# Kernel tuning notes

Hardware: AMD Instinct MI355X
Metric: run time of the kernel (lower is better)

## Reference

```python
import jax, jax.numpy as jnp
import numpy as np
from jax import lax

B, T, S = 8, 4096, 64  # batch, time steps, hidden states


def setup_inputs() -> dict:
    key = jax.random.key(0)
    k1, k2 = jax.random.split(key)
    # log-domain pairwise factors: log_factors[b, t, i, j] = log p(z_{t+1}=j, x_t | z_t=i)
    log_factors = jax.random.normal(k1, (B, T, S, S), dtype=jnp.float32)
    # initial log factor over the first state
    log_init = jax.random.normal(k2, (B, S), dtype=jnp.float32)
    return {"log_factors": log_factors, "log_init": log_init}


def reference(log_factors, log_init):
    """HMM forward algorithm: sequential logaddexp/add chain reduction over time.

    Equivalent to sequential_sum_product(logaddexp, add, log_factors, 'time')
    followed by adding log_init over 'state' and reducing all with logaddexp.
    Implemented as the O(T*S^2) alpha-recursion (vector carry) rather than the
    O(T*S^3) matrix chain -- same math, efficient form.
    """
    fs = jnp.moveaxis(log_factors, 1, 0)  # [T, B, S, S]

    def step(alpha, f_t):
        # alpha: [B, S] over state i ; f_t: [B, S, S] over (i, j)
        alpha_next = jax.nn.logsumexp(alpha[:, :, None] + f_t, axis=1)  # [B, S]
        return alpha_next, None

    alpha_T, _ = lax.scan(step, log_init, fs)
    return jax.nn.logsumexp(alpha_T, axis=-1)  # [B] log-normalizer
```

## Files before the change

kernel.cpp:

```cpp
#include <hip/hip_runtime.h>


#define HMM_B 8
#define HMM_T 4096
#define HMM_S 64
#define HMM_C 128
#define HMM_L (HMM_T / HMM_C)

typedef __attribute__((ext_vector_type(8))) short s16x8;
typedef __attribute__((ext_vector_type(4))) float f32x4;
typedef __attribute__((ext_vector_type(4))) unsigned int u32x4;

__device__ inline void gld16(const float* g, const float* l) {
  __builtin_amdgcn_global_load_lds((const __attribute__((address_space(1))) void*)g,
                                   (__attribute__((address_space(3))) void*)l, 16, 0, 0);
}

__device__ inline unsigned cvtpk(float lo, float hi) {
  unsigned r;
  asm("v_cvt_pk_bf16_f32 %0, %1, %2" : "=v"(r) : "v"(lo), "v"(hi));
  return r;
}

__device__ inline float dpp_fmax16(float x) {
  int xi = __float_as_int(x);
  x = fmaxf(x, __int_as_float(__builtin_amdgcn_mov_dpp(xi, 0xB1, 0xF, 0xF, 1)));
  xi = __float_as_int(x);
  x = fmaxf(x, __int_as_float(__builtin_amdgcn_mov_dpp(xi, 0x4E, 0xF, 0xF, 1)));
  xi = __float_as_int(x);
  x = fmaxf(x, __int_as_float(__builtin_amdgcn_mov_dpp(xi, 0x141, 0xF, 0xF, 1)));
  xi = __float_as_int(x);
  x = fmaxf(x, __int_as_float(__builtin_amdgcn_mov_dpp(xi, 0x140, 0xF, 0xF, 1)));
  return x;
}

__device__ inline float bflo(unsigned w) { return __uint_as_float(w << 16); }
__device__ inline float bfhi(unsigned w) { return __uint_as_float(w & 0xffff0000u); }


__global__ __launch_bounds__(256, 3)
void hmm_phase1(const float* __restrict__ lf, unsigned short* __restrict__ wsE,
                unsigned short* __restrict__ wsEt, float* __restrict__ wsM) {
  __shared__ struct {
    float fbuf[2][4096];
    unsigned short fB[4096];
    unsigned short escr[4][1408];
  } sm;

  const int tid = threadIdx.x;
  const int w   = tid >> 6;
  const int l   = tid & 63;
  const int wg  = blockIdx.x;
  const int bb  = wg >> 7;
  const int cc  = wg & (HMM_C - 1);
  const float* fbase = lf + ((size_t)(bb * HMM_T + cc * HMM_L)) * (HMM_S * HMM_S);

  auto issue = [&](int t) {
    const int par = t & 1;
    const float* fb = fbase + (size_t)t * 4096;
#pragma unroll
    for (int u = 0; u < 4; ++u) {
      int slot = (w * 4 + u) * 64 + l;
      int k    = slot >> 4;
      int q16  = slot & 15;
      const float* src = fb + k * 64 + ((q16 ^ (k & 7)) << 2);
      gld16(src, &sm.fbuf[par][(w * 4 + u) * 256]);
    }
  };

  issue(0);
  issue(1);

  float mracc0 = 0.f, mracc1 = 0.f, mracc2 = 0.f, mracc3 = 0.f;
  const int c4 = l & 15, q = l >> 4;

  for (int t = 0; t < HMM_L; ++t) {
    const int par = t & 1;

    if (t < HMM_L - 1) asm volatile("s_waitcnt vmcnt(4)" ::: "memory");
    else               asm volatile("s_waitcnt vmcnt(0)" ::: "memory");
    __builtin_amdgcn_sched_barrier(0);

#pragma unroll
    for (int u = 0; u < 2; ++u) {
      const int g = 2 * w + (l >> 5);
      const int j = (l & 31) + 32 * u;
      float v[8];
#pragma unroll
      for (int e = 0; e < 8; ++e) {
        int k = 8 * g + e;
        v[e] = sm.fbuf[par][k * 64 + (((j >> 2) ^ (k & 7)) << 2) + (j & 3)];
      }
      unsigned p0 = cvtpk(__expf(v[0]), __expf(v[1]));
      unsigned p1 = cvtpk(__expf(v[2]), __expf(v[3]));
      unsigned p2 = cvtpk(__expf(v[4]), __expf(v[5]));
      unsigned p3 = cvtpk(__expf(v[6]), __expf(v[7]));
      int slot = ((g >> 2) * 4 + (j >> 4)) * 64 + ((g & 3) << 4) + (j & 15);
      u32x4 o; o.x = p0; o.y = p1; o.z = p2; o.w = p3;
      *(u32x4*)&sm.fB[slot * 8] = o;
    }

    asm volatile("s_waitcnt lgkmcnt(0)" ::: "memory");
    __builtin_amdgcn_sched_barrier(0);
    __builtin_amdgcn_s_barrier();
    __builtin_amdgcn_sched_barrier(0);

    if (t + 2 < HMM_L) issue(t + 2);

    s16x8 a0, a1;
    if (t == 0) {
      const int iloc = 16 * w + (l & 15);
      const int kb0 = (l >> 4) * 8, kb1 = 32 + (l >> 4) * 8;
#pragma unroll
      for (int e = 0; e < 8; ++e) {
        a0[e] = (short)((kb0 + e == iloc) ? 0x3F80 : 0);
        a1[e] = (short)((kb1 + e == iloc) ? 0x3F80 : 0);
      }
    } else {
      a0 = *(const s16x8*)&sm.escr[w][(l & 15) * 88 + ((l >> 4) * 8)];
      a1 = *(const s16x8*)&sm.escr[w][(l & 15) * 88 + 32 + ((l >> 4) * 8)];
    }

    f32x4 acc[4];
#pragma unroll
    for (int n = 0; n < 4; ++n) {
      s16x8 b0 = *(const s16x8*)&sm.fB[((0 + n) * 64 + l) * 8];
      s16x8 b1 = *(const s16x8*)&sm.fB[((4 + n) * 64 + l) * 8];
      f32x4 c = {0.f, 0.f, 0.f, 0.f};
      c = __builtin_amdgcn_mfma_f32_16x16x32_bf16(a0, b0, c, 0, 0, 0);
      c = __builtin_amdgcn_mfma_f32_16x16x32_bf16(a1, b1, c, 0, 0, 0);
      acc[n] = c;
    }

    float inv[4];
    {
      float m0 = fmaxf(fmaxf(acc[0][0], acc[1][0]), fmaxf(acc[2][0], acc[3][0]));
      float m1 = fmaxf(fmaxf(acc[0][1], acc[1][1]), fmaxf(acc[2][1], acc[3][1]));
      float m2 = fmaxf(fmaxf(acc[0][2], acc[1][2]), fmaxf(acc[2][2], acc[3][2]));
      float m3 = fmaxf(fmaxf(acc[0][3], acc[1][3]), fmaxf(acc[2][3], acc[3][3]));
      m0 = dpp_fmax16(m0); m1 = dpp_fmax16(m1);
      m2 = dpp_fmax16(m2); m3 = dpp_fmax16(m3);
      mracc0 += __log2f(m0); mracc1 += __log2f(m1);
      mracc2 += __log2f(m2); mracc3 += __log2f(m3);
      inv[0] = __builtin_amdgcn_rcpf(m0); inv[1] = __builtin_amdgcn_rcpf(m1);
      inv[2] = __builtin_amdgcn_rcpf(m2); inv[3] = __builtin_amdgcn_rcpf(m3);
    }
#pragma unroll
    for (int n = 0; n < 4; ++n) {
      unsigned p0 = cvtpk(acc[n][0] * inv[0], acc[n][1] * inv[1]);
      unsigned p1 = cvtpk(acc[n][2] * inv[2], acc[n][3] * inv[3]);
      sm.escr[w][(4 * q + 0) * 88 + 16 * n + c4] = (unsigned short)(p0 & 0xffffu);
      sm.escr[w][(4 * q + 1) * 88 + 16 * n + c4] = (unsigned short)(p0 >> 16);
      sm.escr[w][(4 * q + 2) * 88 + 16 * n + c4] = (unsigned short)(p1 & 0xffffu);
      sm.escr[w][(4 * q + 3) * 88 + 16 * n + c4] = (unsigned short)(p1 >> 16);
    }

    asm volatile("s_waitcnt lgkmcnt(0)" ::: "memory");
    __builtin_amdgcn_sched_barrier(0);
    __builtin_amdgcn_s_barrier();
    __builtin_amdgcn_sched_barrier(0);
  }

  __syncthreads();

  {
    const size_t cb = ((size_t)(bb * HMM_C + cc)) * 4096;
    const int j = tid & 63, p4 = tid >> 6;
    unsigned short o0[8], o1[8];
#pragma unroll
    for (int rl = 0; rl < 8; ++rl)  o0[rl] = sm.escr[p4][rl * 88 + j];
#pragma unroll
    for (int rl = 0; rl < 8; ++rl)  o1[rl] = sm.escr[p4][(rl + 8) * 88 + j];
    *(u32x4*)&wsEt[cb + j * 64 + p4 * 16]     = *(u32x4*)o0;
    *(u32x4*)&wsEt[cb + j * 64 + p4 * 16 + 8] = *(u32x4*)o1;

    if ((cc & 15) == 0) {
      const int r = tid >> 2, jq = tid & 3;
      u32x4 v0 = *(const u32x4*)&sm.escr[r >> 4][(r & 15) * 88 + jq * 16];
      u32x4 v1 = *(const u32x4*)&sm.escr[r >> 4][(r & 15) * 88 + jq * 16 + 8];
      *(u32x4*)&wsE[cb + r * 64 + jq * 16]     = v0;
      *(u32x4*)&wsE[cb + r * 64 + jq * 16 + 8] = v1;
    }

    if (c4 == 0) {
      const float ln2 = 0.6931471805599453f;
      float* dst = wsM + (size_t)(bb * HMM_C + cc) * 64 + 16 * w + 4 * q;
      dst[0] = mracc0 * ln2; dst[1] = mracc1 * ln2;
      dst[2] = mracc2 * ln2; dst[3] = mracc3 * ln2;
    }
  }
}


__global__ __launch_bounds__(64)
void hmm_combine16(const unsigned short* __restrict__ inE,
                   const unsigned short* __restrict__ inEt,
                   const float* __restrict__ inM,
                   unsigned short* __restrict__ outEt,
                   float* __restrict__ outM) {
  __shared__ float sS[64];
  __shared__ float sM[64];
  __shared__ unsigned short pL[4096];

  const int l = threadIdx.x, c4 = l & 15, q = l >> 4;
  const int b = blockIdx.x >> 3, g = blockIdx.x & 7;
  const int cbase = b * HMM_C + g * 16;

  s16x8 afr[4][2];
#pragma unroll
  for (int m = 0; m < 4; ++m)
#pragma unroll
    for (int h = 0; h < 2; ++h)
      afr[m][h] = *(const s16x8*)&inE[(size_t)cbase * 4096 +
                                      (m * 16 + c4) * 64 + h * 32 + q * 8];
  sM[l] = inM[(size_t)cbase * 64 + l];

  u32x4 braw[2][4];
  float mv;
  {
    const unsigned short* Et = inEt + (size_t)(cbase + 1) * 4096;
#pragma unroll
    for (int h = 0; h < 2; ++h)
#pragma unroll
      for (int n = 0; n < 4; ++n)
        braw[h][n] = *(const u32x4*)&Et[(n * 16 + c4) * 64 + h * 32 + q * 8];
    mv = inM[(size_t)(cbase + 1) * 64 + l];
  }

  for (int c = 1; c < 16; ++c) {
    u32x4 bcur[2][4];
#pragma unroll
    for (int h = 0; h < 2; ++h)
#pragma unroll
      for (int n = 0; n < 4; ++n) bcur[h][n] = braw[h][n];
    float mcur = mv;
    if (c < 15) {
      const unsigned short* Et = inEt + (size_t)(cbase + c + 1) * 4096;
#pragma unroll
      for (int h = 0; h < 2; ++h)
#pragma unroll
        for (int n = 0; n < 4; ++n)
          braw[h][n] = *(const u32x4*)&Et[(n * 16 + c4) * 64 + h * 32 + q * 8];
      mv = inM[(size_t)(cbase + c + 1) * 64 + l];
    }

    float nu = mcur;
    nu = fmaxf(nu, __shfl_xor(nu, 1));  nu = fmaxf(nu, __shfl_xor(nu, 2));
    nu = fmaxf(nu, __shfl_xor(nu, 4));  nu = fmaxf(nu, __shfl_xor(nu, 8));
    nu = fmaxf(nu, __shfl_xor(nu, 16)); nu = fmaxf(nu, __shfl_xor(nu, 32));
    sS[l] = __expf(mcur - nu);

    s16x8 bfr[2][4];
#pragma unroll
    for (int h = 0; h < 2; ++h) {
      f32x4 s0 = *(const f32x4*)&sS[h * 32 + q * 8];
      f32x4 s1 = *(const f32x4*)&sS[h * 32 + q * 8 + 4];
#pragma unroll
      for (int n = 0; n < 4; ++n) {
        u32x4 raw = bcur[h][n];
        unsigned p0 = cvtpk(bflo(raw.x) * s0[0], bfhi(raw.x) * s0[1]);
        unsigned p1 = cvtpk(bflo(raw.y) * s0[2], bfhi(raw.y) * s0[3]);
        unsigned p2 = cvtpk(bflo(raw.z) * s1[0], bfhi(raw.z) * s1[1]);
        unsigned p3 = cvtpk(bflo(raw.w) * s1[2], bfhi(raw.w) * s1[3]);
        u32x4 o; o.x = p0; o.y = p1; o.z = p2; o.w = p3;
        bfr[h][n] = *(s16x8*)&o;
      }
    }

    f32x4 acc[4][4];
#pragma unroll
    for (int m = 0; m < 4; ++m)
#pragma unroll
      for (int n = 0; n < 4; ++n) {
        f32x4 cc2 = {0.f, 0.f, 0.f, 0.f};
        cc2 = __builtin_amdgcn_mfma_f32_16x16x32_bf16(afr[m][0], bfr[0][n], cc2, 0, 0, 0);
        cc2 = __builtin_amdgcn_mfma_f32_16x16x32_bf16(afr[m][1], bfr[1][n], cc2, 0, 0, 0);
        acc[m][n] = cc2;
      }

    float rmax[4][4];
#pragma unroll
    for (int m = 0; m < 4; ++m)
#pragma unroll
      for (int r = 0; r < 4; ++r) {
        float v = fmaxf(fmaxf(acc[m][0][r], acc[m][1][r]),
                        fmaxf(acc[m][2][r], acc[m][3][r]));
        v = fmaxf(v, __shfl_xor(v, 1));
        v = fmaxf(v, __shfl_xor(v, 2));
        v = fmaxf(v, __shfl_xor(v, 4));
        v = fmaxf(v, __shfl_xor(v, 8));
        rmax[m][r] = v;
      }
    if (c4 == 0) {
#pragma unroll
      for (int m = 0; m < 4; ++m)
#pragma unroll
        for (int r = 0; r < 4; ++r)
          sM[16 * m + 4 * q + r] += nu + __logf(rmax[m][r]);
    }

    if (c < 15) {
#pragma unroll
      for (int m = 0; m < 4; ++m) {
        float i0 = __builtin_amdgcn_rcpf(rmax[m][0]);
        float i1 = __builtin_amdgcn_rcpf(rmax[m][1]);
        float i2 = __builtin_amdgcn_rcpf(rmax[m][2]);
        float i3 = __builtin_amdgcn_rcpf(rmax[m][3]);
#pragma unroll
        for (int n = 0; n < 4; ++n) {
          unsigned p01 = cvtpk(acc[m][n][0] * i0, acc[m][n][1] * i1);
          unsigned p23 = cvtpk(acc[m][n][2] * i2, acc[m][n][3] * i3);
          pL[(16 * m + 4 * q + 0) * 64 + 16 * n + c4] = (unsigned short)(p01 & 0xffffu);
          pL[(16 * m + 4 * q + 1) * 64 + 16 * n + c4] = (unsigned short)(p01 >> 16);
          pL[(16 * m + 4 * q + 2) * 64 + 16 * n + c4] = (unsigned short)(p23 & 0xffffu);
          pL[(16 * m + 4 * q + 3) * 64 + 16 * n + c4] = (unsigned short)(p23 >> 16);
        }
      }
#pragma unroll
      for (int m = 0; m < 4; ++m)
#pragma unroll
        for (int h = 0; h < 2; ++h)
          afr[m][h] = *(const s16x8*)&pL[(m * 16 + c4) * 64 + h * 32 + q * 8];
    } else {
      const size_t oi = (size_t)(b * 8 + g) * 4096;
#pragma unroll
      for (int m = 0; m < 4; ++m) {
        float i0 = __builtin_amdgcn_rcpf(rmax[m][0]);
        float i1 = __builtin_amdgcn_rcpf(rmax[m][1]);
        float i2 = __builtin_amdgcn_rcpf(rmax[m][2]);
        float i3 = __builtin_amdgcn_rcpf(rmax[m][3]);
#pragma unroll
        for (int n = 0; n < 4; ++n) {
          unsigned p01 = cvtpk(acc[m][n][0] * i0, acc[m][n][1] * i1);
          unsigned p23 = cvtpk(acc[m][n][2] * i2, acc[m][n][3] * i3);
          unsigned long long packed = (unsigned long long)p01 |
                                      ((unsigned long long)p23 << 32);
          *(unsigned long long*)&outEt[oi + (16 * n + c4) * 64 + 16 * m + 4 * q] = packed;
        }
      }
      outM[(size_t)(b * 8 + g) * 64 + l] = sM[l];
    }
  }
}


__device__ inline float rdlane(float v, int t) {
  return __int_as_float(__builtin_amdgcn_readlane(__float_as_int(v), t));
}

__global__ __launch_bounds__(64)
void hmm_final(const unsigned short* __restrict__ Et, const float* __restrict__ M,
               const float* __restrict__ linit, float* __restrict__ out) {
  const int b = blockIdx.x, l = threadIdx.x;
  float alpha = linit[b * 64 + l];

  int4 e[8]; float mg;
  {
    const int4* src = (const int4*)(Et + (size_t)(b * 8) * 4096 + (size_t)l * 64);
#pragma unroll
    for (int u = 0; u < 8; ++u) e[u] = src[u];
    mg = M[(size_t)(b * 8) * 64 + l];
  }

  for (int g = 0; g < 8; ++g) {
    int4 ec[8];
#pragma unroll
    for (int u = 0; u < 8; ++u) ec[u] = e[u];
    float mcur = mg;
    if (g < 7) {
      const int4* src = (const int4*)(Et + (size_t)(b * 8 + g + 1) * 4096 + (size_t)l * 64);
#pragma unroll
      for (int u = 0; u < 8; ++u) e[u] = src[u];
      mg = M[(size_t)(b * 8 + g + 1) * 64 + l];
    }

    float av = alpha + mcur;
    float mx = av;
    mx = fmaxf(mx, __shfl_xor(mx, 1));  mx = fmaxf(mx, __shfl_xor(mx, 2));
    mx = fmaxf(mx, __shfl_xor(mx, 4));  mx = fmaxf(mx, __shfl_xor(mx, 8));
    mx = fmaxf(mx, __shfl_xor(mx, 16)); mx = fmaxf(mx, __shfl_xor(mx, 32));
    float wv = __expf(av - mx);
    float s = 0.f;
#pragma unroll
    for (int u = 0; u < 8; ++u) {
      unsigned w0 = (unsigned)ec[u].x, w1 = (unsigned)ec[u].y;
      unsigned w2 = (unsigned)ec[u].z, w3 = (unsigned)ec[u].w;
      s = fmaf(rdlane(wv, 8 * u + 0), bflo(w0), s);
      s = fmaf(rdlane(wv, 8 * u + 1), bfhi(w0), s);
      s = fmaf(rdlane(wv, 8 * u + 2), bflo(w1), s);
      s = fmaf(rdlane(wv, 8 * u + 3), bfhi(w1), s);
      s = fmaf(rdlane(wv, 8 * u + 4), bflo(w2), s);
      s = fmaf(rdlane(wv, 8 * u + 5), bfhi(w2), s);
      s = fmaf(rdlane(wv, 8 * u + 6), bflo(w3), s);
      s = fmaf(rdlane(wv, 8 * u + 7), bfhi(w3), s);
    }
    alpha = mx + __logf(s);
  }

  float mx = alpha;
  mx = fmaxf(mx, __shfl_xor(mx, 1));  mx = fmaxf(mx, __shfl_xor(mx, 2));
  mx = fmaxf(mx, __shfl_xor(mx, 4));  mx = fmaxf(mx, __shfl_xor(mx, 8));
  mx = fmaxf(mx, __shfl_xor(mx, 16)); mx = fmaxf(mx, __shfl_xor(mx, 32));
  float s = __expf(alpha - mx);
  s += __shfl_xor(s, 1);  s += __shfl_xor(s, 2);  s += __shfl_xor(s, 4);
  s += __shfl_xor(s, 8);  s += __shfl_xor(s, 16); s += __shfl_xor(s, 32);
  if (l == 0) out[b] = mx + __logf(s);
}

extern "C" void kernel_launch(void* const* d_in, const int* in_sizes, int n_in,
                              void* d_out, int out_size, void* d_ws, size_t ws_size,
                              hipStream_t stream) {
  (void)in_sizes; (void)n_in; (void)out_size; (void)ws_size;
  const float* lf    = (const float*)d_in[0];
  const float* linit = (const float*)d_in[1];
  float* out = (float*)d_out;

  unsigned short* E_A  = (unsigned short*)d_ws;
  unsigned short* Et_A = E_A + (size_t)1024 * 4096;
  float*          M_A  = (float*)(Et_A + (size_t)1024 * 4096);
  unsigned short* Et_B = (unsigned short*)(M_A + (size_t)1024 * 64);
  float*          M_B  = (float*)(Et_B + (size_t)64 * 4096);

  hmm_phase1<<<dim3(HMM_B * HMM_C), dim3(256), 0, stream>>>(lf, E_A, Et_A, M_A);
  hmm_combine16<<<dim3(64), dim3(64), 0, stream>>>(E_A, Et_A, M_A, Et_B, M_B);
  hmm_final<<<dim3(HMM_B), dim3(64), 0, stream>>>(Et_B, M_B, linit, out);
}
```

Baseline: 229.2 us.

## Double-buffer phase1 B tile, drop one barrier, merge combine and final into one kernel

Phase1 now double-buffers the exponentiated bf16 factor tile, which lets it drop the second per-step barrier and issue the next global load at the top of each step instead of after the barrier. Occupancy hint goes from 3 to 2 blocks because of the larger LDS footprint. The combine16 and final kernels are replaced by one 512-thread reduce kernel per batch: each of 8 waves folds 16 chunk matrices starting from an identity, then a tree of MFMA products merges them, and the init vector is applied at the end. This removes a launch and the separate E output write, at the cost of a serial tree tail and lower phase1 occupancy.

Measured after the change: 235.9 us. 1.03x slower.

```diff
diff --git a/kernel.cpp b/kernel.cpp
--- a/kernel.cpp
+++ b/kernel.cpp
@@ -38,12 +38,12 @@
 __device__ inline float bfhi(unsigned w) { return __uint_as_float(w & 0xffff0000u); }
 
 
-__global__ __launch_bounds__(256, 3)
-void hmm_phase1(const float* __restrict__ lf, unsigned short* __restrict__ wsE,
-                unsigned short* __restrict__ wsEt, float* __restrict__ wsM) {
+__global__ __launch_bounds__(256, 2)
+void hmm_phase1(const float* __restrict__ lf, unsigned short* __restrict__ wsEt,
+                float* __restrict__ wsM) {
   __shared__ struct {
     float fbuf[2][4096];
-    unsigned short fB[4096];
+    unsigned short fB[2][4096];
     unsigned short escr[4][1408];
   } sm;
 
@@ -69,13 +69,13 @@
   };
 
   issue(0);
-  issue(1);
 
   float mracc0 = 0.f, mracc1 = 0.f, mracc2 = 0.f, mracc3 = 0.f;
   const int c4 = l & 15, q = l >> 4;
 
   for (int t = 0; t < HMM_L; ++t) {
     const int par = t & 1;
+    if (t + 1 < HMM_L) issue(t + 1);
 
     if (t < HMM_L - 1) asm volatile("s_waitcnt vmcnt(4)" ::: "memory");
     else               asm volatile("s_waitcnt vmcnt(0)" ::: "memory");
@@ -97,15 +97,12 @@
       unsigned p3 = cvtpk(__expf(v[6]), __expf(v[7]));
       int slot = ((g >> 2) * 4 + (j >> 4)) * 64 + ((g & 3) << 4) + (j & 15);
       u32x4 o; o.x = p0; o.y = p1; o.z = p2; o.w = p3;
-      *(u32x4*)&sm.fB[slot * 8] = o;
+      *(u32x4*)&sm.fB[par][slot * 8] = o;
     }
 
     asm volatile("s_waitcnt lgkmcnt(0)" ::: "memory");
     __builtin_amdgcn_sched_barrier(0);
     __builtin_amdgcn_s_barrier();
-    __builtin_amdgcn_sched_barrier(0);
-
-    if (t + 2 < HMM_L) issue(t + 2);
 
     s16x8 a0, a1;
     if (t == 0) {
@@ -124,8 +121,8 @@
     f32x4 acc[4];
 #pragma unroll
     for (int n = 0; n < 4; ++n) {
-      s16x8 b0 = *(const s16x8*)&sm.fB[((0 + n) * 64 + l) * 8];
-      s16x8 b1 = *(const s16x8*)&sm.fB[((4 + n) * 64 + l) * 8];
+      s16x8 b0 = *(const s16x8*)&sm.fB[par][((0 + n) * 64 + l) * 8];
+      s16x8 b1 = *(const s16x8*)&sm.fB[par][((4 + n) * 64 + l) * 8];
       f32x4 c = {0.f, 0.f, 0.f, 0.f};
       c = __builtin_amdgcn_mfma_f32_16x16x32_bf16(a0, b0, c, 0, 0, 0);
       c = __builtin_amdgcn_mfma_f32_16x16x32_bf16(a1, b1, c, 0, 0, 0);
@@ -154,14 +151,7 @@
       sm.escr[w][(4 * q + 2) * 88 + 16 * n + c4] = (unsigned short)(p1 & 0xffffu);
       sm.escr[w][(4 * q + 3) * 88 + 16 * n + c4] = (unsigned short)(p1 >> 16);
     }
-
-    asm volatile("s_waitcnt lgkmcnt(0)" ::: "memory");
-    __builtin_amdgcn_sched_barrier(0);
-    __builtin_amdgcn_s_barrier();
-    __builtin_amdgcn_sched_barrier(0);
   }
-
-  __syncthreads();
 
   {
     const size_t cb = ((size_t)(bb * HMM_C + cc)) * 4096;
@@ -173,14 +163,6 @@
     for (int rl = 0; rl < 8; ++rl)  o1[rl] = sm.escr[p4][(rl + 8) * 88 + j];
     *(u32x4*)&wsEt[cb + j * 64 + p4 * 16]     = *(u32x4*)o0;
     *(u32x4*)&wsEt[cb + j * 64 + p4 * 16 + 8] = *(u32x4*)o1;
-
-    if ((cc & 15) == 0) {
-      const int r = tid >> 2, jq = tid & 3;
-      u32x4 v0 = *(const u32x4*)&sm.escr[r >> 4][(r & 15) * 88 + jq * 16];
-      u32x4 v1 = *(const u32x4*)&sm.escr[r >> 4][(r & 15) * 88 + jq * 16 + 8];
-      *(u32x4*)&wsE[cb + r * 64 + jq * 16]     = v0;
-      *(u32x4*)&wsE[cb + r * 64 + jq * 16 + 8] = v1;
-    }
 
     if (c4 == 0) {
       const float ln2 = 0.6931471805599453f;
@@ -192,69 +174,47 @@
 }
 
 
-__global__ __launch_bounds__(64)
-void hmm_combine16(const unsigned short* __restrict__ inE,
-                   const unsigned short* __restrict__ inEt,
-                   const float* __restrict__ inM,
-                   unsigned short* __restrict__ outEt,
-                   float* __restrict__ outM) {
-  __shared__ float sS[64];
-  __shared__ float sM[64];
-  __shared__ unsigned short pL[4096];
-
-  const int l = threadIdx.x, c4 = l & 15, q = l >> 4;
-  const int b = blockIdx.x >> 3, g = blockIdx.x & 7;
-  const int cbase = b * HMM_C + g * 16;
+#define PMS 72
+
+__global__ __launch_bounds__(512)
+void hmm_reduce(const unsigned short* __restrict__ Et, const float* __restrict__ M,
+                const float* __restrict__ linit, float* __restrict__ out) {
+  __shared__ unsigned short pmat[8][PMS * 64];
+  __shared__ float pm[8][64];
+  __shared__ float sS[8][64];
+  __shared__ float sLin[64];
+  __shared__ float sW[64];
+
+  const int tid = threadIdx.x;
+  const int v = tid >> 6, l = tid & 63, c4 = l & 15, q = l >> 4;
+  const int b = blockIdx.x;
+
+  if (tid < 64) sLin[tid] = linit[b * 64 + tid];
+  pm[v][l] = 0.0f;
 
   s16x8 afr[4][2];
 #pragma unroll
   for (int m = 0; m < 4; ++m)
 #pragma unroll
     for (int h = 0; h < 2; ++h)
-      afr[m][h] = *(const s16x8*)&inE[(size_t)cbase * 4096 +
-                                      (m * 16 + c4) * 64 + h * 32 + q * 8];
-  sM[l] = inM[(size_t)cbase * 64 + l];
-
-  u32x4 braw[2][4];
-  float mv;
-  {
-    const unsigned short* Et = inEt + (size_t)(cbase + 1) * 4096;
-#pragma unroll
-    for (int h = 0; h < 2; ++h)
-#pragma unroll
-      for (int n = 0; n < 4; ++n)
-        braw[h][n] = *(const u32x4*)&Et[(n * 16 + c4) * 64 + h * 32 + q * 8];
-    mv = inM[(size_t)(cbase + 1) * 64 + l];
-  }
-
-  for (int c = 1; c < 16; ++c) {
-    u32x4 bcur[2][4];
-#pragma unroll
-    for (int h = 0; h < 2; ++h)
-#pragma unroll
-      for (int n = 0; n < 4; ++n) bcur[h][n] = braw[h][n];
-    float mcur = mv;
-    if (c < 15) {
-      const unsigned short* Et = inEt + (size_t)(cbase + c + 1) * 4096;
-#pragma unroll
-      for (int h = 0; h < 2; ++h)
-#pragma unroll
-        for (int n = 0; n < 4; ++n)
-          braw[h][n] = *(const u32x4*)&Et[(n * 16 + c4) * 64 + h * 32 + q * 8];
-      mv = inM[(size_t)(cbase + c + 1) * 64 + l];
-    }
-
+#pragma unroll
+      for (int e = 0; e < 8; ++e)
+        afr[m][h][e] = (short)((32 * h + 8 * q + e == 16 * m + c4) ? 0x3F80 : 0);
+
+  f32x4 acc[4][4];
+  float rmax[4][4];
+
+  auto fold = [&](u32x4 (&bcur)[2][4], float mcur, float* pmAcc, float* sSv) {
     float nu = mcur;
     nu = fmaxf(nu, __shfl_xor(nu, 1));  nu = fmaxf(nu, __shfl_xor(nu, 2));
     nu = fmaxf(nu, __shfl_xor(nu, 4));  nu = fmaxf(nu, __shfl_xor(nu, 8));
     nu = fmaxf(nu, __shfl_xor(nu, 16)); nu = fmaxf(nu, __shfl_xor(nu, 32));
-    sS[l] = __expf(mcur - nu);
-
+    sSv[l] = __expf(mcur - nu);
     s16x8 bfr[2][4];
 #pragma unroll
     for (int h = 0; h < 2; ++h) {
-      f32x4 s0 = *(const f32x4*)&sS[h * 32 + q * 8];
-      f32x4 s1 = *(const f32x4*)&sS[h * 32 + q * 8 + 4];
+      f32x4 s0 = *(const f32x4*)&sSv[h * 32 + q * 8];
+      f32x4 s1 = *(const f32x4*)&sSv[h * 32 + q * 8 + 4];
 #pragma unroll
       for (int n = 0; n < 4; ++n) {
         u32x4 raw = bcur[h][n];
@@ -266,145 +226,199 @@
         bfr[h][n] = *(s16x8*)&o;
       }
     }
-
-    f32x4 acc[4][4];
-#pragma unroll
-    for (int m = 0; m < 4; ++m)
-#pragma unroll
-      for (int n = 0; n < 4; ++n) {
-        f32x4 cc2 = {0.f, 0.f, 0.f, 0.f};
-        cc2 = __builtin_amdgcn_mfma_f32_16x16x32_bf16(afr[m][0], bfr[0][n], cc2, 0, 0, 0);
-        cc2 = __builtin_amdgcn_mfma_f32_16x16x32_bf16(afr[m][1], bfr[1][n], cc2, 0, 0, 0);
-        acc[m][n] = cc2;
-      }
-
-    float rmax[4][4];
+#pragma unroll
+    for (int m = 0; m < 4; ++m)
+#pragma unroll
+      for (int n = 0; n < 4; ++n) {
+        f32x4 c = {0.f, 0.f, 0.f, 0.f};
+        c = __builtin_amdgcn_mfma_f32_16x16x32_bf16(afr[m][0], bfr[0][n], c, 0, 0, 0);
+        c = __builtin_amdgcn_mfma_f32_16x16x32_bf16(afr[m][1], bfr[1][n], c, 0, 0, 0);
+        acc[m][n] = c;
+      }
 #pragma unroll
     for (int m = 0; m < 4; ++m)
 #pragma unroll
       for (int r = 0; r < 4; ++r) {
-        float v = fmaxf(fmaxf(acc[m][0][r], acc[m][1][r]),
+        float x = fmaxf(fmaxf(acc[m][0][r], acc[m][1][r]),
                         fmaxf(acc[m][2][r], acc[m][3][r]));
-        v = fmaxf(v, __shfl_xor(v, 1));
-        v = fmaxf(v, __shfl_xor(v, 2));
-        v = fmaxf(v, __shfl_xor(v, 4));
-        v = fmaxf(v, __shfl_xor(v, 8));
-        rmax[m][r] = v;
+        x = fmaxf(x, __shfl_xor(x, 1));
+        x = fmaxf(x, __shfl_xor(x, 2));
+        x = fmaxf(x, __shfl_xor(x, 4));
+        x = fmaxf(x, __shfl_xor(x, 8));
+        rmax[m][r] = fmaxf(x, 1e-30f);
       }
     if (c4 == 0) {
 #pragma unroll
       for (int m = 0; m < 4; ++m)
 #pragma unroll
         for (int r = 0; r < 4; ++r)
-          sM[16 * m + 4 * q + r] += nu + __logf(rmax[m][r]);
-    }
-
-    if (c < 15) {
-#pragma unroll
-      for (int m = 0; m < 4; ++m) {
-        float i0 = __builtin_amdgcn_rcpf(rmax[m][0]);
-        float i1 = __builtin_amdgcn_rcpf(rmax[m][1]);
-        float i2 = __builtin_amdgcn_rcpf(rmax[m][2]);
-        float i3 = __builtin_amdgcn_rcpf(rmax[m][3]);
-#pragma unroll
-        for (int n = 0; n < 4; ++n) {
-          unsigned p01 = cvtpk(acc[m][n][0] * i0, acc[m][n][1] * i1);
-          unsigned p23 = cvtpk(acc[m][n][2] * i2, acc[m][n][3] * i3);
-          pL[(16 * m + 4 * q + 0) * 64 + 16 * n + c4] = (unsigned short)(p01 & 0xffffu);
-          pL[(16 * m + 4 * q + 1) * 64 + 16 * n + c4] = (unsigned short)(p01 >> 16);
-          pL[(16 * m + 4 * q + 2) * 64 + 16 * n + c4] = (unsigned short)(p23 & 0xffffu);
-          pL[(16 * m + 4 * q + 3) * 64 + 16 * n + c4] = (unsigned short)(p23 >> 16);
-        }
-      }
-#pragma unroll
-      for (int m = 0; m < 4; ++m)
+          pmAcc[16 * m + 4 * q + r] += nu + __logf(rmax[m][r]);
+    }
+  };
+
+  auto roundtrip = [&](unsigned short* ps) {
+#pragma unroll
+    for (int m = 0; m < 4; ++m) {
+      float i0 = __builtin_amdgcn_rcpf(rmax[m][0]);
+      float i1 = __builtin_amdgcn_rcpf(rmax[m][1]);
+      float i2 = __builtin_amdgcn_rcpf(rmax[m][2]);
+      float i3 = __builtin_amdgcn_rcpf(rmax[m][3]);
+#pragma unroll
+      for (int n = 0; n < 4; ++n) {
+        unsigned p01 = cvtpk(acc[m][n][0] * i0, acc[m][n][1] * i1);
+        unsigned p23 = cvtpk(acc[m][n][2] * i2, acc[m][n][3] * i3);
+        ps[(16 * m + 4 * q + 0) * PMS + 16 * n + c4] = (unsigned short)(p01 & 0xffffu);
+        ps[(16 * m + 4 * q + 1) * PMS + 16 * n + c4] = (unsigned short)(p01 >> 16);
+        ps[(16 * m + 4 * q + 2) * PMS + 16 * n + c4] = (unsigned short)(p23 & 0xffffu);
+        ps[(16 * m + 4 * q + 3) * PMS + 16 * n + c4] = (unsigned short)(p23 >> 16);
+      }
+    }
+#pragma unroll
+    for (int m = 0; m < 4; ++m)
+#pragma unroll
+      for (int h = 0; h < 2; ++h)
+        afr[m][h] = *(const s16x8*)&ps[(16 * m + c4) * PMS + 32 * h + 8 * q];
+  };
+
+  auto storeEt = [&](unsigned short* pd) {
+#pragma unroll
+    for (int m = 0; m < 4; ++m) {
+      float i0 = __builtin_amdgcn_rcpf(rmax[m][0]);
+      float i1 = __builtin_amdgcn_rcpf(rmax[m][1]);
+      float i2 = __builtin_amdgcn_rcpf(rmax[m][2]);
+      float i3 = __builtin_amdgcn_rcpf(rmax[m][3]);
+#pragma unroll
+      for (int n = 0; n < 4; ++n) {
+        unsigned p01 = cvtpk(acc[m][n][0] * i0, acc[m][n][1] * i1);
+        unsigned p23 = cvtpk(acc[m][n][2] * i2, acc[m][n][3] * i3);
+        unsigned long long packed = (unsigned long long)p01 |
+                                    ((unsigned long long)p23 << 32);
+        *(unsigned long long*)&pd[(16 * n + c4) * PMS + 16 * m + 4 * q] = packed;
+      }
+    }
+  };
+
+  {
+    const int cidx0 = b * HMM_C + 16 * v;
+    u32x4 braw[2][4];
+    float mv;
+#pragma unroll
+    for (int h = 0; h < 2; ++h)
+#pragma unroll
+      for (int n = 0; n < 4; ++n)
+        braw[h][n] = *(const u32x4*)&Et[(size_t)cidx0 * 4096 +
+                                        (16 * n + c4) * 64 + 32 * h + 8 * q];
+    mv = M[(size_t)cidx0 * 64 + l];
+
+    for (int c = 0; c < 16; ++c) {
+      u32x4 bcur[2][4];
+#pragma unroll
+      for (int h = 0; h < 2; ++h)
+#pragma unroll
+        for (int n = 0; n < 4; ++n) bcur[h][n] = braw[h][n];
+      float mcur = mv;
+      if (c < 15) {
+        const size_t cb = (size_t)(cidx0 + c + 1) * 4096;
 #pragma unroll
         for (int h = 0; h < 2; ++h)
-          afr[m][h] = *(const s16x8*)&pL[(m * 16 + c4) * 64 + h * 32 + q * 8];
-    } else {
-      const size_t oi = (size_t)(b * 8 + g) * 4096;
-#pragma unroll
-      for (int m = 0; m < 4; ++m) {
-        float i0 = __builtin_amdgcn_rcpf(rmax[m][0]);
-        float i1 = __builtin_amdgcn_rcpf(rmax[m][1]);
-        float i2 = __builtin_amdgcn_rcpf(rmax[m][2]);
-        float i3 = __builtin_amdgcn_rcpf(rmax[m][3]);
-#pragma unroll
-        for (int n = 0; n < 4; ++n) {
-          unsigned p01 = cvtpk(acc[m][n][0] * i0, acc[m][n][1] * i1);
-          unsigned p23 = cvtpk(acc[m][n][2] * i2, acc[m][n][3] * i3);
-          unsigned long long packed = (unsigned long long)p01 |
-                                      ((unsigned long long)p23 << 32);
-          *(unsigned long long*)&outEt[oi + (16 * n + c4) * 64 + 16 * m + 4 * q] = packed;
-        }
-      }
-      outM[(size_t)(b * 8 + g) * 64 + l] = sM[l];
+#pragma unroll
+          for (int n = 0; n < 4; ++n)
+            braw[h][n] = *(const u32x4*)&Et[cb + (16 * n + c4) * 64 + 32 * h + 8 * q];
+        mv = M[(size_t)(cidx0 + c + 1) * 64 + l];
+      }
+      fold(bcur, mcur, pm[v], sS[v]);
+      if (c < 15) roundtrip(pmat[v]);
+      else        storeEt(pmat[v]);
     }
   }
-}
-
-
-__device__ inline float rdlane(float v, int t) {
-  return __int_as_float(__builtin_amdgcn_readlane(__float_as_int(v), t));
-}
-
-__global__ __launch_bounds__(64)
-void hmm_final(const unsigned short* __restrict__ Et, const float* __restrict__ M,
-               const float* __restrict__ linit, float* __restrict__ out) {
-  const int b = blockIdx.x, l = threadIdx.x;
-  float alpha = linit[b * 64 + l];
-
-  int4 e[8]; float mg;
-  {
-    const int4* src = (const int4*)(Et + (size_t)(b * 8) * 4096 + (size_t)l * 64);
-#pragma unroll
-    for (int u = 0; u < 8; ++u) e[u] = src[u];
-    mg = M[(size_t)(b * 8) * 64 + l];
+  __syncthreads();
+
+  if (v < 2) {
+    const int sb = 4 * v;
+#pragma unroll
+    for (int m = 0; m < 4; ++m)
+#pragma unroll
+      for (int h = 0; h < 2; ++h)
+#pragma unroll
+        for (int e = 0; e < 8; ++e)
+          afr[m][h][e] = (short)pmat[sb][(32 * h + 8 * q + e) * PMS + 16 * m + c4];
+    for (int c = 1; c < 4; ++c) {
+      u32x4 bcur[2][4];
+#pragma unroll
+      for (int h = 0; h < 2; ++h)
+#pragma unroll
+        for (int n = 0; n < 4; ++n)
+          bcur[h][n] = *(const u32x4*)&pmat[sb + c][(16 * n + c4) * PMS + 32 * h + 8 * q];
+      float mcur = pm[sb + c][l];
+      fold(bcur, mcur, pm[sb], sS[v]);
+      if (v == 0)      roundtrip(pmat[0]);
+      else if (c < 3)  roundtrip(pmat[4]);
+      else             storeEt(pmat[4]);
+    }
   }
-
-  for (int g = 0; g < 8; ++g) {
-    int4 ec[8];
-#pragma unroll
-    for (int u = 0; u < 8; ++u) ec[u] = e[u];
-    float mcur = mg;
-    if (g < 7) {
-      const int4* src = (const int4*)(Et + (size_t)(b * 8 + g + 1) * 4096 + (size_t)l * 64);
-#pragma unroll
-      for (int u = 0; u < 8; ++u) e[u] = src[u];
-      mg = M[(size_t)(b * 8 + g + 1) * 64 + l];
-    }
-
-    float av = alpha + mcur;
-    float mx = av;
+  __syncthreads();
+
+  if (v == 0) {
+    u32x4 bcur[2][4];
+#pragma unroll
+    for (int h = 0; h < 2; ++h)
+#pragma unroll
+      for (int n = 0; n < 4; ++n)
+        bcur[h][n] = *(const u32x4*)&pmat[4][(16 * n + c4) * PMS + 32 * h + 8 * q];
+    float mcur = pm[4][l];
+
+    float nu = mcur;
+    nu = fmaxf(nu, __shfl_xor(nu, 1));  nu = fmaxf(nu, __shfl_xor(nu, 2));
+    nu = fmaxf(nu, __shfl_xor(nu, 4));  nu = fmaxf(nu, __shfl_xor(nu, 8));
+    nu = fmaxf(nu, __shfl_xor(nu, 16)); nu = fmaxf(nu, __shfl_xor(nu, 32));
+    sS[0][l] = __expf(mcur - nu);
+    s16x8 bfr[2][4];
+#pragma unroll
+    for (int h = 0; h < 2; ++h) {
+      f32x4 s0 = *(const f32x4*)&sS[0][h * 32 + q * 8];
+      f32x4 s1 = *(const f32x4*)&sS[0][h * 32 + q * 8 + 4];
+#pragma unroll
+      for (int n = 0; n < 4; ++n) {
+        u32x4 raw = bcur[h][n];
+        unsigned p0 = cvtpk(bflo(raw.x) * s0[0], bfhi(raw.x) * s0[1]);
+        unsigned p1 = cvtpk(bflo(raw.y) * s0[2], bfhi(raw.y) * s0[3]);
+        unsigned p2 = cvtpk(bflo(raw.z) * s1[0], bfhi(raw.z) * s1[1]);
+        unsigned p3 = cvtpk(bflo(raw.w) * s1[2], bfhi(raw.w) * s1[3]);
+        u32x4 o; o.x = p0; o.y = p1; o.z = p2; o.w = p3;
+        bfr[h][n] = *(s16x8*)&o;
+      }
+    }
+#pragma unroll
+    for (int m = 0; m < 4; ++m)
+#pragma unroll
+      for (int n = 0; n < 4; ++n) {
+        f32x4 c = {0.f, 0.f, 0.f, 0.f};
+        c = __builtin_amdgcn_mfma_f32_16x16x32_bf16(afr[m][0], bfr[0][n], c, 0, 0, 0);
+        c = __builtin_amdgcn_mfma_f32_16x16x32_bf16(afr[m][1], bfr[1][n], c, 0, 0, 0);
+        acc[m][n] = c;
+      }
+
+    float tv = sLin[l] + pm[0][l];
+    float mx = tv;
     mx = fmaxf(mx, __shfl_xor(mx, 1));  mx = fmaxf(mx, __shfl_xor(mx, 2));
     mx = fmaxf(mx, __shfl_xor(mx, 4));  mx = fmaxf(mx, __shfl_xor(mx, 8));
     mx = fmaxf(mx, __shfl_xor(mx, 16)); mx = fmaxf(mx, __shfl_xor(mx, 32));
-    float wv = __expf(av - mx);
-    float s = 0.f;
-#pragma unroll
-    for (int u = 0; u < 8; ++u) {
-      unsigned w0 = (unsigned)ec[u].x, w1 = (unsigned)ec[u].y;
-      unsigned w2 = (unsigned)ec[u].z, w3 = (unsigned)ec[u].w;
-      s = fmaf(rdlane(wv, 8 * u + 0), bflo(w0), s);
-      s = fmaf(rdlane(wv, 8 * u + 1), bfhi(w0), s);
-      s = fmaf(rdlane(wv, 8 * u + 2), bflo(w1), s);
-      s = fmaf(rdlane(wv, 8 * u + 3), bfhi(w1), s);
-      s = fmaf(rdlane(wv, 8 * u + 4), bflo(w2), s);
-      s = fmaf(rdlane(wv, 8 * u + 5), bfhi(w2), s);
-      s = fmaf(rdlane(wv, 8 * u + 6), bflo(w3), s);
-      s = fmaf(rdlane(wv, 8 * u + 7), bfhi(w3), s);
-    }
-    alpha = mx + __logf(s);
+    sW[l] = __expf(tv - mx);
+
+    float tot = 0.f;
+#pragma unroll
+    for (int m = 0; m < 4; ++m)
+#pragma unroll
+      for (int r = 0; r < 4; ++r) {
+        float rs = acc[m][0][r] + acc[m][1][r] + acc[m][2][r] + acc[m][3][r];
+        rs += __shfl_xor(rs, 1); rs += __shfl_xor(rs, 2);
+        rs += __shfl_xor(rs, 4); rs += __shfl_xor(rs, 8);
+        if (c4 == 0) tot += sW[16 * m + 4 * q + r] * rs;
+      }
+    tot += __shfl_xor(tot, 16);
+    tot += __shfl_xor(tot, 32);
+    if (l == 0) out[b] = mx + nu + __logf(tot);
   }
-
-  float mx = alpha;
-  mx = fmaxf(mx, __shfl_xor(mx, 1));  mx = fmaxf(mx, __shfl_xor(mx, 2));
-  mx = fmaxf(mx, __shfl_xor(mx, 4));  mx = fmaxf(mx, __shfl_xor(mx, 8));
-  mx = fmaxf(mx, __shfl_xor(mx, 16)); mx = fmaxf(mx, __shfl_xor(mx, 32));
-  float s = __expf(alpha - mx);
-  s += __shfl_xor(s, 1);  s += __shfl_xor(s, 2);  s += __shfl_xor(s, 4);
-  s += __shfl_xor(s, 8);  s += __shfl_xor(s, 16); s += __shfl_xor(s, 32);
-  if (l == 0) out[b] = mx + __logf(s);
 }
 
 extern "C" void kernel_launch(void* const* d_in, const int* in_sizes, int n_in,
@@ -415,13 +429,9 @@
   const float* linit = (const float*)d_in[1];
   float* out = (float*)d_out;
 
-  unsigned short* E_A  = (unsigned short*)d_ws;
-  unsigned short* Et_A = E_A + (size_t)1024 * 4096;
+  unsigned short* Et_A = (unsigned short*)d_ws;
   float*          M_A  = (float*)(Et_A + (size_t)1024 * 4096);
-  unsigned short* Et_B = (unsigned short*)(M_A + (size_t)1024 * 64);
-  float*          M_B  = (float*)(Et_B + (size_t)64 * 4096);
-
-  hmm_phase1<<<dim3(HMM_B * HMM_C), dim3(256), 0, stream>>>(lf, E_A, Et_A, M_A);
-  hmm_combine16<<<dim3(64), dim3(64), 0, stream>>>(E_A, Et_A, M_A, Et_B, M_B);
-  hmm_final<<<dim3(HMM_B), dim3(64), 0, stream>>>(Et_B, M_B, linit, out);
-}
+
+  hmm_phase1<<<dim3(HMM_B * HMM_C), dim3(256), 0, stream>>>(lf, Et_A, M_A);
+  hmm_reduce<<<dim3(HMM_B), dim3(512), 0, stream>>>(Et_A, M_A, linit, out);
+}
```
